# Kernel tuning notes

Measured on AMD Instinct MI355X. Metric: run time of the kernel, lower is better.

The kernel has to match this reference:

```python
import jax, jax.numpy as jnp
import numpy as np

BASE_DIM = 512
NUM_HEADS = 4
HEAD_DIM = BASE_DIM // NUM_HEADS
NUM_USERS = 100000
TIMESLOTS = 24
B, S = 64, 512


def setup_inputs() -> dict:
    key = jax.random.key(0)
    ks = jax.random.split(key, 16)
    timeslot_embedded = jax.random.normal(ks[0], (TIMESLOTS, BASE_DIM), jnp.float32)
    smoothed_timeslot_embedded = jax.random.normal(ks[1], (TIMESLOTS, BASE_DIM), jnp.float32)
    user_embedded = jax.random.normal(ks[2], (B, BASE_DIM), jnp.float32)
    user_x = jax.random.randint(ks[3], (B,), 0, NUM_USERS)
    hour_x = jax.random.randint(ks[4], (B, S), 0, TIMESLOTS)
    hour_mask = jax.random.randint(ks[5], (B, S, TIMESLOTS), 0, 2)
    # guarantee no row is fully masked (avoids all -inf softmax rows)
    hour_mask = hour_mask.at[:, :, 0].set(0)
    sc = 0.02
    user_pref_table = jax.random.normal(ks[6], (NUM_USERS, BASE_DIM), jnp.float32) * sc
    Wq = jax.random.normal(ks[7], (NUM_HEADS, HEAD_DIM, 2 * BASE_DIM), jnp.float32) * sc
    bq = jnp.zeros((NUM_HEADS, HEAD_DIM), jnp.float32)
    Wk = jax.random.normal(ks[8], (NUM_HEADS, HEAD_DIM, BASE_DIM), jnp.float32) * sc
    bk = jnp.zeros((NUM_HEADS, HEAD_DIM), jnp.float32)
    Wv = jax.random.normal(ks[9], (NUM_HEADS, HEAD_DIM, BASE_DIM), jnp.float32) * sc
    bv = jnp.zeros((NUM_HEADS, HEAD_DIM), jnp.float32)
    W_unify = jax.random.normal(ks[10], (BASE_DIM, BASE_DIM), jnp.float32) * sc
    b_unify = jnp.zeros((BASE_DIM,), jnp.float32)
    W_time = jax.random.normal(ks[11], (TIMESLOTS, BASE_DIM), jnp.float32) * sc
    b_time = jnp.zeros((TIMESLOTS,), jnp.float32)
    return dict(timeslot_embedded=timeslot_embedded,
                smoothed_timeslot_embedded=smoothed_timeslot_embedded,
                user_embedded=user_embedded,
                user_x=user_x, hour_x=hour_x, hour_mask=hour_mask,
                user_pref_table=user_pref_table,
                Wq=Wq, bq=bq, Wk=Wk, bk=bk, Wv=Wv, bv=bv,
                W_unify=W_unify, b_unify=b_unify,
                W_time=W_time, b_time=b_time)


def reference(timeslot_embedded, smoothed_timeslot_embedded, user_embedded,
              user_x, hour_x, hour_mask, user_pref_table,
              Wq, bq, Wk, bk, Wv, bv, W_unify, b_unify, W_time, b_time):
    b, s = hour_x.shape
    n = b * s
    hour = hour_x.reshape(n)                                  # [N]
    mask = hour_mask.reshape(n, TIMESLOTS)                    # [N, 24]

    # user preference broadcast over sequence, then flattened
    up = user_pref_table[user_x]                              # [B, D]
    user_feature = jnp.broadcast_to(up[:, None, :], (b, s, BASE_DIM)).reshape(n, BASE_DIM)
    time_feature = timeslot_embedded[hour]                    # [N, D]
    query = jnp.concatenate([user_feature, time_feature], axis=-1)  # [N, 2D]

    # all heads batched (equivalent to the per-head Python loop + concat)
    q = jnp.einsum('nd,hed->nhe', query, Wq) + bq             # [N, H, E]
    k = jnp.einsum('kd,hed->khe', timeslot_embedded, Wk) + bk # [24, H, E]
    v = jnp.einsum('kd,hed->khe', timeslot_embedded, Wv) + bv # [24, H, E]

    scale = 1.0 / jnp.sqrt(jnp.float32(HEAD_DIM))
    scores = jnp.einsum('nhe,khe->nhk', q, k) * scale         # [N, H, 24]
    scores = jnp.where(mask[:, None, :] == 1, -jnp.inf, scores)
    attn = jax.nn.softmax(scores, axis=-1)
    out = jnp.einsum('nhk,khe->nhe', attn, v).reshape(n, BASE_DIM)  # concat heads

    head_outputs = out.reshape(b, s, BASE_DIM)
    at_emb = head_outputs @ W_unify.T + b_unify               # [B, S, D]
    time_logits = head_outputs @ W_time.T + b_time            # [B, S, 24]
    return at_emb, time_logits
```

## Files before the change

### kernel.cpp

```cpp
#include <hip/hip_runtime.h>
#include <hip/hip_bf16.h>
#include <math.h>

#define TS   24
#define NH   4
#define HD   128
#define D    512
#define NB   64
#define SEQ  512
#define NTOT (NB*SEQ)

typedef __bf16 bf16;
typedef __bf16 bf16x8 __attribute__((ext_vector_type(8)));
typedef float  f32x4  __attribute__((ext_vector_type(4)));

#define OFF_QU  0
#define OFF_QT  32768
#define OFF_K   45056
#define OFF_V   57344
#define OFF_SU  69632
#define OFF_ST  75776
#define OFF_BSW 78080

__global__ __launch_bounds__(256) void k1_proj(
    const float* __restrict__ timeslot, const int* __restrict__ user_x,
    const float* __restrict__ upt,
    const float* __restrict__ Wq, const float* __restrict__ bq,
    const float* __restrict__ Wk, const float* __restrict__ bk,
    const float* __restrict__ Wv, const float* __restrict__ bv,
    float* __restrict__ ws)
{
    int tau = blockIdx.x * 256 + threadIdx.x;
    if (tau < 32768) {
        int he = tau >> 6, b = tau & 63;
        const float4* wrow = (const float4*)(Wq + (size_t)he * 1024);
        int u = user_x[b];
        const float4* urow = (const float4*)(upt + (size_t)u * 512);
        float acc = bq[he];
        #pragma unroll 4
        for (int d = 0; d < 128; ++d) {
            float4 w = wrow[d], x = urow[d];
            acc += w.x*x.x + w.y*x.y + w.z*x.z + w.w*x.w;
        }
        ws[OFF_QU + b*512 + he] = acc;
    } else if (tau < 69632) {
        int idx = tau - 32768;
        int sec = idx / 12288;
        int r   = idx % 12288;
        int he  = r / 24, t = r % 24;
        const float* wbase; float bias; int outoff;
        if (sec == 0)      { wbase = Wq + (size_t)he*1024 + 512; bias = 0.f;    outoff = OFF_QT; }
        else if (sec == 1) { wbase = Wk + (size_t)he*512;        bias = bk[he]; outoff = OFF_K;  }
        else               { wbase = Wv + (size_t)he*512;        bias = bv[he]; outoff = OFF_V;  }
        const float4* w4 = (const float4*)wbase;
        const float4* x4 = (const float4*)(timeslot + t*512);
        float acc = bias;
        #pragma unroll 4
        for (int d = 0; d < 128; ++d) {
            float4 w = w4[d], x = x4[d];
            acc += w.x*x.x + w.y*x.y + w.z*x.z + w.w*x.w;
        }
        ws[outoff + t*512 + he] = acc;
    }
}

static __device__ __forceinline__ float dot128(const float* __restrict__ a,
                                               const float* __restrict__ b) {
    const float4* a4 = (const float4*)a;
    const float4* b4 = (const float4*)b;
    float acc = 0.f;
    #pragma unroll 8
    for (int i = 0; i < 32; ++i) {
        float4 x = a4[i], y = b4[i];
        acc += x.x*y.x + x.y*y.y + x.z*y.z + x.w*y.w;
    }
    return acc;
}

__global__ __launch_bounds__(256) void k2_small(
    const float* __restrict__ Wu, const float* __restrict__ Wt,
    float* __restrict__ ws)
{
    const float SCL = 1.4426950408889634f / sqrtf(128.0f);
    int tau = blockIdx.x * 256 + threadIdx.x;
    bf16* Bsw = (bf16*)(ws + OFF_BSW);
    if (tau < 6144) {
        int kk = tau % 24, h = (tau / 24) & 3, b = tau / 96;
        float acc = dot128(ws + OFF_QU + b*512 + h*128, ws + OFF_K + kk*512 + h*128);
        ws[OFF_SU + tau] = acc * SCL;
    } else if (tau < 8448) {
        int i = tau - 6144;
        int kk = i % 24, h = (i / 24) & 3, t = i / 96;
        float acc = dot128(ws + OFF_QT + t*512 + h*128, ws + OFF_K + kk*512 + h*128);
        ws[OFF_ST + i] = acc * SCL;
    } else if (tau < 57600) {
        int i = tau - 8448;
        int c = i & 511, r96 = i >> 9;
        int h = r96 / 24, kk = r96 % 24;
        float acc = dot128(ws + OFF_V + kk*512 + h*128, Wu + (size_t)c*512 + h*128);
        Bsw[((r96 >> 3)*544 + c)*8 + (r96 & 7)] = (bf16)acc;
    } else if (tau < 59904) {
        int i = tau - 57600;
        int j = i % 24, r96 = i / 24;
        int h = r96 / 24, kk = r96 % 24;
        float acc = dot128(ws + OFF_V + kk*512 + h*128, Wt + (size_t)j*512 + h*128);
        Bsw[((r96 >> 3)*544 + 512 + j)*8 + (r96 & 7)] = (bf16)acc;
    } else if (tau < 60672) {
        int i = tau - 59904;
        int g = i >> 6, rem = i & 63;
        int c = 536 + (rem >> 3), j = rem & 7;
        Bsw[(g*544 + c)*8 + j] = (bf16)0.f;
    }
}

__global__ __launch_bounds__(256) void k3_main(
    const int* __restrict__ hour_x, const int* __restrict__ hour_mask,
    const float* __restrict__ b_unify, const float* __restrict__ b_time,
    const float* __restrict__ ws, float* __restrict__ out)
{
    __shared__ int  maskL[64 * 24];
    __shared__ int  hourL[64];
    __shared__ __align__(16) bf16 attnL[64][104];

    int tid = threadIdx.x;
    int n0  = blockIdx.x * 64;
    int b   = n0 >> 9;

    for (int i = tid; i < 64 * 24; i += 256)
        maskL[i] = hour_mask[(size_t)n0 * 24 + i];
    if (tid < 64) hourL[tid] = hour_x[n0 + tid];
    __syncthreads();

    {
        int h = tid >> 6, row = tid & 63;
        int t = hourL[row];
        const float* su = ws + OFF_SU + (b*4 + h)*24;
        const float* st = ws + OFF_ST + (t*4 + h)*24;
        const int*   m  = maskL + row*24;
        float w[24]; float sum = 0.f;
        #pragma unroll
        for (int kk = 0; kk < 24; ++kk) {
            float e = exp2f(su[kk] + st[kk]);
            e = m[kk] ? 0.f : e;
            w[kk] = e; sum += e;
        }
        float inv = 1.f / sum;
        #pragma unroll
        for (int kk = 0; kk < 24; ++kk)
            attnL[row][h*24 + kk] = (bf16)(w[kk] * inv);
    }
    __syncthreads();

    const bf16* Bsw = (const bf16*)(ws + OFF_BSW);
    int wv = tid >> 6, l = tid & 63;
    int quad = l >> 4, cl = l & 15;
    int rowA = wv*16 + cl;

    bf16x8 a0 = *(const bf16x8*)&attnL[rowA][ 0 + quad*8];
    bf16x8 a1 = *(const bf16x8*)&attnL[rowA][32 + quad*8];
    bf16x8 a2 = *(const bf16x8*)&attnL[rowA][64 + quad*8];

    float* tl_out = out + (size_t)NTOT * 512;

    for (int ct = 0; ct < 34; ++ct) {
        int col = ct*16 + cl;
        const bf16* bp = Bsw + ((size_t)(quad*544 + col)) * 8;
        f32x4 acc = {0.f, 0.f, 0.f, 0.f};
        acc = __builtin_amdgcn_mfma_f32_16x16x32_bf16(a0, *(const bf16x8*)(bp),              acc, 0, 0, 0);
        acc = __builtin_amdgcn_mfma_f32_16x16x32_bf16(a1, *(const bf16x8*)(bp + 4*544*8),    acc, 0, 0, 0);
        acc = __builtin_amdgcn_mfma_f32_16x16x32_bf16(a2, *(const bf16x8*)(bp + 8*544*8),    acc, 0, 0, 0);
        int nbase = n0 + wv*16 + quad*4;
        if (col < 512) {
            float bias = b_unify[col];
            #pragma unroll
            for (int r = 0; r < 4; ++r)
                out[(size_t)(nbase + r)*512 + col] = acc[r] + bias;
        } else {
            int cc = col - 512;
            if (cc < 24) {
                float bias = b_time[cc];
                #pragma unroll
                for (int r = 0; r < 4; ++r)
                    tl_out[(size_t)(nbase + r)*24 + cc] = acc[r] + bias;
            }
        }
    }
}

extern "C" void kernel_launch(void* const* d_in, const int* in_sizes, int n_in,
                              void* d_out, int out_size, void* d_ws, size_t ws_size,
                              hipStream_t stream) {
    const float* timeslot = (const float*)d_in[0];
    const int*   user_x   = (const int*)d_in[3];
    const int*   hour_x   = (const int*)d_in[4];
    const int*   hour_mask= (const int*)d_in[5];
    const float* upt      = (const float*)d_in[6];
    const float* Wq       = (const float*)d_in[7];
    const float* bq       = (const float*)d_in[8];
    const float* Wk       = (const float*)d_in[9];
    const float* bk       = (const float*)d_in[10];
    const float* Wv       = (const float*)d_in[11];
    const float* bv       = (const float*)d_in[12];
    const float* Wu       = (const float*)d_in[13];
    const float* b_unify  = (const float*)d_in[14];
    const float* Wt       = (const float*)d_in[15];
    const float* b_time   = (const float*)d_in[16];

    float* ws  = (float*)d_ws;
    float* out = (float*)d_out;

    k1_proj <<<272, 256, 0, stream>>>(timeslot, user_x, upt, Wq, bq, Wk, bk, Wv, bv, ws);
    k2_small<<<237, 256, 0, stream>>>(Wu, Wt, ws);
    k3_main <<<512, 256, 0, stream>>>(hour_x, hour_mask, b_unify, b_time, ws, out);
}
```

Measured before the change: 344.4 us.

## Process 128 rows per block in k3 with two MFMA tiles sharing B loads

The main kernel now handles 128 rows per block instead of 64, halving the grid to 256 blocks. Each wave computes two 16-row tiles, so every B fragment loaded from the workspace feeds two MFMAs. The mask copy is vectorised to int4 loads, and the time-logit columns are split into their own loop, which removes the per-iteration branch. The cost is fewer blocks (256 on a GPU with many CUs) and higher register and LDS use per block, so there is less parallelism for hiding the latency of the store-bound output writes.

```diff
diff --git a/kernel.cpp b/kernel.cpp
--- a/kernel.cpp
+++ b/kernel.cpp
@@ -118,21 +118,28 @@
     const float* __restrict__ b_unify, const float* __restrict__ b_time,
     const float* __restrict__ ws, float* __restrict__ out)
 {
-    __shared__ int  maskL[64 * 24];
-    __shared__ int  hourL[64];
-    __shared__ __align__(16) bf16 attnL[64][104];
+    __shared__ int  maskL[128 * 24];
+    __shared__ int  hourL[128];
+    __shared__ __align__(16) bf16 attnL[128][104];
 
     int tid = threadIdx.x;
-    int n0  = blockIdx.x * 64;
+    int n0  = blockIdx.x * 128;
     int b   = n0 >> 9;
 
-    for (int i = tid; i < 64 * 24; i += 256)
-        maskL[i] = hour_mask[(size_t)n0 * 24 + i];
-    if (tid < 64) hourL[tid] = hour_x[n0 + tid];
+    {
+        const int4* src = (const int4*)(hour_mask + (size_t)n0 * 24);
+        int4* dst = (int4*)maskL;
+        #pragma unroll
+        for (int i = tid; i < 128 * 24 / 4; i += 256)
+            dst[i] = src[i];
+        if (tid < 128) hourL[tid] = hour_x[n0 + tid];
+    }
     __syncthreads();
 
-    {
-        int h = tid >> 6, row = tid & 63;
+    #pragma unroll
+    for (int it = 0; it < 2; ++it) {
+        int task = tid + it * 256;
+        int h = task >> 7, row = task & 127;
         int t = hourL[row];
         const float* su = ws + OFF_SU + (b*4 + h)*24;
         const float* st = ws + OFF_ST + (t*4 + h)*24;
@@ -154,34 +161,62 @@
     const bf16* Bsw = (const bf16*)(ws + OFF_BSW);
     int wv = tid >> 6, l = tid & 63;
     int quad = l >> 4, cl = l & 15;
-    int rowA = wv*16 + cl;
-
-    bf16x8 a0 = *(const bf16x8*)&attnL[rowA][ 0 + quad*8];
-    bf16x8 a1 = *(const bf16x8*)&attnL[rowA][32 + quad*8];
-    bf16x8 a2 = *(const bf16x8*)&attnL[rowA][64 + quad*8];
-
-    float* tl_out = out + (size_t)NTOT * 512;
-
-    for (int ct = 0; ct < 34; ++ct) {
+    int r0 = wv*32 + cl;
+    int r1 = r0 + 16;
+
+    bf16x8 a00 = *(const bf16x8*)&attnL[r0][ 0 + quad*8];
+    bf16x8 a01 = *(const bf16x8*)&attnL[r0][32 + quad*8];
+    bf16x8 a02 = *(const bf16x8*)&attnL[r0][64 + quad*8];
+    bf16x8 a10 = *(const bf16x8*)&attnL[r1][ 0 + quad*8];
+    bf16x8 a11 = *(const bf16x8*)&attnL[r1][32 + quad*8];
+    bf16x8 a12 = *(const bf16x8*)&attnL[r1][64 + quad*8];
+
+    int nbase = n0 + wv*32 + quad*4;
+
+    for (int ct = 0; ct < 32; ++ct) {
         int col = ct*16 + cl;
         const bf16* bp = Bsw + ((size_t)(quad*544 + col)) * 8;
-        f32x4 acc = {0.f, 0.f, 0.f, 0.f};
-        acc = __builtin_amdgcn_mfma_f32_16x16x32_bf16(a0, *(const bf16x8*)(bp),              acc, 0, 0, 0);
-        acc = __builtin_amdgcn_mfma_f32_16x16x32_bf16(a1, *(const bf16x8*)(bp + 4*544*8),    acc, 0, 0, 0);
-        acc = __builtin_amdgcn_mfma_f32_16x16x32_bf16(a2, *(const bf16x8*)(bp + 8*544*8),    acc, 0, 0, 0);
-        int nbase = n0 + wv*16 + quad*4;
-        if (col < 512) {
-            float bias = b_unify[col];
+        bf16x8 b0 = *(const bf16x8*)(bp);
+        bf16x8 b1 = *(const bf16x8*)(bp + 4*544*8);
+        bf16x8 b2 = *(const bf16x8*)(bp + 8*544*8);
+        f32x4 acc0 = {0.f, 0.f, 0.f, 0.f};
+        f32x4 acc1 = {0.f, 0.f, 0.f, 0.f};
+        acc0 = __builtin_amdgcn_mfma_f32_16x16x32_bf16(a00, b0, acc0, 0, 0, 0);
+        acc1 = __builtin_amdgcn_mfma_f32_16x16x32_bf16(a10, b0, acc1, 0, 0, 0);
+        acc0 = __builtin_amdgcn_mfma_f32_16x16x32_bf16(a01, b1, acc0, 0, 0, 0);
+        acc1 = __builtin_amdgcn_mfma_f32_16x16x32_bf16(a11, b1, acc1, 0, 0, 0);
+        acc0 = __builtin_amdgcn_mfma_f32_16x16x32_bf16(a02, b2, acc0, 0, 0, 0);
+        acc1 = __builtin_amdgcn_mfma_f32_16x16x32_bf16(a12, b2, acc1, 0, 0, 0);
+        float bias = b_unify[col];
+        #pragma unroll
+        for (int r = 0; r < 4; ++r) {
+            out[(size_t)(nbase + r)*512 + col]      = acc0[r] + bias;
+            out[(size_t)(nbase + 16 + r)*512 + col] = acc1[r] + bias;
+        }
+    }
+
+    float* tl_out = out + (size_t)NTOT * 512;
+    for (int ct = 32; ct < 34; ++ct) {
+        int col = ct*16 + cl;
+        int cc  = col - 512;
+        const bf16* bp = Bsw + ((size_t)(quad*544 + col)) * 8;
+        bf16x8 b0 = *(const bf16x8*)(bp);
+        bf16x8 b1 = *(const bf16x8*)(bp + 4*544*8);
+        bf16x8 b2 = *(const bf16x8*)(bp + 8*544*8);
+        f32x4 acc0 = {0.f, 0.f, 0.f, 0.f};
+        f32x4 acc1 = {0.f, 0.f, 0.f, 0.f};
+        acc0 = __builtin_amdgcn_mfma_f32_16x16x32_bf16(a00, b0, acc0, 0, 0, 0);
+        acc1 = __builtin_amdgcn_mfma_f32_16x16x32_bf16(a10, b0, acc1, 0, 0, 0);
+        acc0 = __builtin_amdgcn_mfma_f32_16x16x32_bf16(a01, b1, acc0, 0, 0, 0);
+        acc1 = __builtin_amdgcn_mfma_f32_16x16x32_bf16(a11, b1, acc1, 0, 0, 0);
+        acc0 = __builtin_amdgcn_mfma_f32_16x16x32_bf16(a02, b2, acc0, 0, 0, 0);
+        acc1 = __builtin_amdgcn_mfma_f32_16x16x32_bf16(a12, b2, acc1, 0, 0, 0);
+        if (cc < 24) {
+            float bias = b_time[cc];
             #pragma unroll
-            for (int r = 0; r < 4; ++r)
-                out[(size_t)(nbase + r)*512 + col] = acc[r] + bias;
-        } else {
-            int cc = col - 512;
-            if (cc < 24) {
-                float bias = b_time[cc];
-                #pragma unroll
-                for (int r = 0; r < 4; ++r)
-                    tl_out[(size_t)(nbase + r)*24 + cc] = acc[r] + bias;
+            for (int r = 0; r < 4; ++r) {
+                tl_out[(size_t)(nbase + r)*24 + cc]      = acc0[r] + bias;
+                tl_out[(size_t)(nbase + 16 + r)*24 + cc] = acc1[r] + bias;
             }
         }
     }
@@ -211,5 +246,5 @@
 
     k1_proj <<<272, 256, 0, stream>>>(timeslot, user_x, upt, Wq, bq, Wk, bk, Wv, bv, ws);
     k2_small<<<237, 256, 0, stream>>>(Wu, Wt, ws);
-    k3_main <<<512, 256, 0, stream>>>(hour_x, hour_mask, b_unify, b_time, ws, out);
-}
+    k3_main <<<256, 256, 0, stream>>>(hour_x, hour_mask, b_unify, b_time, ws, out);
+}
```

New measurement: 344.3 us. No clear change (-0.0%).
